# Kernel tuning notes

Hardware: AMD Instinct MI355X
Metric: run time of the kernel (lower is better)

Reference implementation:

```python
import jax, jax.numpy as jnp
import numpy as np
import math

D_MODEL = 768
N_HEAD = 12
SEQ_LEN = 2048
BATCH = 4


def setup_inputs() -> dict:
    key = jax.random.key(0)
    ks = jax.random.split(key, 5)
    x = jax.random.normal(ks[0], (BATCH, SEQ_LEN, D_MODEL), dtype=jnp.float32)
    s = 1.0 / math.sqrt(D_MODEL)
    W_attn = jax.random.uniform(ks[1], (D_MODEL, 3 * D_MODEL), minval=-s, maxval=s, dtype=jnp.float32)
    b_attn = jax.random.uniform(ks[2], (3 * D_MODEL,), minval=-s, maxval=s, dtype=jnp.float32)
    W_proj = jax.random.uniform(ks[3], (D_MODEL, D_MODEL), minval=-s, maxval=s, dtype=jnp.float32)
    b_proj = jax.random.uniform(ks[4], (D_MODEL,), minval=-s, maxval=s, dtype=jnp.float32)
    return {"x": x, "W_attn": W_attn, "b_attn": b_attn, "W_proj": W_proj, "b_proj": b_proj}


def reference(x, W_attn, b_attn, W_proj, b_proj):
    B, T, C = x.shape
    H = N_HEAD
    hd = C // H
    qkv = x @ W_attn + b_attn  # [B,T,3C]
    q, k, v = jnp.split(qkv, 3, axis=-1)
    # [B,H,T,hd]
    q = q.reshape(B, T, H, hd).transpose(0, 2, 1, 3)
    k = k.reshape(B, T, H, hd).transpose(0, 2, 1, 3)
    v = v.reshape(B, T, H, hd).transpose(0, 2, 1, 3)
    att = jnp.einsum('bhqd,bhkd->bhqk', q, k) * (1.0 / math.sqrt(hd))  # [B,H,T,T]
    causal = jnp.tril(jnp.ones((T, T), dtype=bool))
    att = jnp.where(causal[None, None, :, :], att, -jnp.inf)
    att = jax.nn.softmax(att, axis=-1)
    # attn_pdrop = resid_pdrop = 0.0 -> dropout is identity
    y = jnp.einsum('bhqk,bhkd->bhqd', att, v)  # [B,H,T,hd]
    y = y.transpose(0, 2, 1, 3).reshape(B, T, C)
    return y @ W_proj + b_proj
```

## Files before the change

kernel.cpp:

```cpp
#include <hip/hip_runtime.h>
#include <hip/hip_bf16.h>
#include <math.h>

#define D_MODEL 768
#define N_HEAD  12
#define SEQ     2048
#define BATCH   4
#define HD      64
#define BH      (BATCH*N_HEAD)

typedef __bf16 bf16;
typedef __bf16 bf16x4 __attribute__((ext_vector_type(4)));
typedef __bf16 bf16x8 __attribute__((ext_vector_type(8)));
typedef float  f32x4  __attribute__((ext_vector_type(4)));
typedef float  f32x16 __attribute__((ext_vector_type(16)));
typedef unsigned int u32;

__device__ __forceinline__ f32x4 mfma16(bf16x8 a, bf16x8 b, f32x4 c) {
    return __builtin_amdgcn_mfma_f32_16x16x32_bf16(a, b, c, 0, 0, 0);
}
__device__ __forceinline__ f32x16 mfma32(bf16x8 a, bf16x8 b, f32x16 c) {
    return __builtin_amdgcn_mfma_f32_32x32x16_bf16(a, b, c, 0, 0, 0);
}

__device__ __forceinline__ void gload16(const void* g, void* l) {
    __builtin_amdgcn_global_load_lds((const __attribute__((address_space(1))) u32*)g,
                                     (__attribute__((address_space(3))) u32*)l, 16, 0, 0);
}

__global__ void cvt_bf16(const float* __restrict__ in, bf16* __restrict__ out, int n) {
    int i = (blockIdx.x * blockDim.x + threadIdx.x) * 4;
    if (i < n) {
        float4 v = *(const float4*)(in + i);
        bf16x4 o;
        o[0] = (bf16)v.x; o[1] = (bf16)v.y; o[2] = (bf16)v.z; o[3] = (bf16)v.w;
        *(bf16x4*)(out + i) = o;
    }
}

__global__ __launch_bounds__(256)
void transpose_cvt(const float* __restrict__ in, bf16* __restrict__ out, int R, int C) {
    __shared__ float tile[64][65];
    int tid = threadIdx.x;
    int tr = blockIdx.y * 64, tc = blockIdx.x * 64;
    int r0 = tid >> 4, c0 = (tid & 15) * 4;
    #pragma unroll
    for (int i = 0; i < 4; ++i) {
        float4 v = *(const float4*)&in[(long)(tr + r0 + i * 16) * C + tc + c0];
        tile[r0 + i * 16][c0 + 0] = v.x;
        tile[r0 + i * 16][c0 + 1] = v.y;
        tile[r0 + i * 16][c0 + 2] = v.z;
        tile[r0 + i * 16][c0 + 3] = v.w;
    }
    __syncthreads();
    int orr = (tid & 15) * 4;
    #pragma unroll
    for (int i = 0; i < 4; ++i) {
        int oc = (tid >> 4) + i * 16;
        bf16x4 o;
        #pragma unroll
        for (int j = 0; j < 4; ++j) o[j] = (bf16)tile[orr + j][oc];
        *(bf16x4*)&out[(long)(tc + oc) * R + tr + orr] = o;
    }
}

template<int MODE>
__global__ __launch_bounds__(256)
void gemm_bt(const bf16* __restrict__ A, const bf16* __restrict__ Bt,
             const float* __restrict__ bias,
             bf16* __restrict__ qo, bf16* __restrict__ ko, bf16* __restrict__ vto,
             float* __restrict__ outf,
             int M, int N, int K) {
    __shared__ bf16 As[128 * 32];
    __shared__ bf16 Bs[128 * 32];
    int tid = threadIdx.x;
    int wave = tid >> 6, lane = tid & 63;
    int wr = wave >> 1, wc = wave & 1;
    int lq = lane >> 4, lc = lane & 15;
    int mbase = blockIdx.x * 128, nbase = blockIdx.y * 128;
    int srow = wave * 32 + (lane >> 2), scol = (lane & 3) * 8;
    const bf16* aS = A  + (long)(mbase + srow) * K + scol;
    const bf16* bS = Bt + (long)(nbase + srow) * K + scol;
    char* AsB = (char*)As + wave * 2048;
    char* BsB = (char*)Bs + wave * 2048;
    f32x4 acc[4][4] = {};
    for (int kt = 0; kt < K; kt += 32) {
        gload16(aS + kt,                AsB);
        gload16(aS + 16 * (long)K + kt, AsB + 1024);
        gload16(bS + kt,                BsB);
        gload16(bS + 16 * (long)K + kt, BsB + 1024);
        __syncthreads();
        bf16x8 af[4], bfr[4];
        #pragma unroll
        for (int mf = 0; mf < 4; ++mf)
            af[mf]  = *(const bf16x8*)((char*)As + (wr * 64 + mf * 16 + lc) * 64 + lq * 16);
        #pragma unroll
        for (int nf = 0; nf < 4; ++nf)
            bfr[nf] = *(const bf16x8*)((char*)Bs + (wc * 64 + nf * 16 + lc) * 64 + lq * 16);
        __builtin_amdgcn_s_setprio(1);
        #pragma unroll
        for (int mf = 0; mf < 4; ++mf)
            #pragma unroll
            for (int nf = 0; nf < 4; ++nf)
                acc[mf][nf] = mfma16(af[mf], bfr[nf], acc[mf][nf]);
        __builtin_amdgcn_s_setprio(0);
        __syncthreads();
    }
    #pragma unroll
    for (int mf = 0; mf < 4; ++mf) {
        #pragma unroll
        for (int nf = 0; nf < 4; ++nf) {
            int n = nbase + wc * 64 + nf * 16 + lc;
            float bv = bias[n];
            int m0 = mbase + wr * 64 + mf * 16 + lq * 4;
            if (MODE == 0) {
                int sect = n / 768, cc = n % 768;
                int h = cc >> 6, d = cc & 63;
                int b = m0 >> 11, t0 = m0 & 2047;
                long bh = (long)b * N_HEAD + h;
                if (sect == 0) {
                    #pragma unroll
                    for (int r = 0; r < 4; ++r)
                        qo[(bh * SEQ + t0 + r) * HD + d] = (bf16)((acc[mf][nf][r] + bv) * 0.18033688f);
                } else if (sect == 1) {
                    #pragma unroll
                    for (int r = 0; r < 4; ++r)
                        ko[(bh * SEQ + t0 + r) * HD + d] = (bf16)(acc[mf][nf][r] + bv);
                } else {
                    bf16x4 o;
                    #pragma unroll
                    for (int r = 0; r < 4; ++r) o[r] = (bf16)(acc[mf][nf][r] + bv);
                    *(bf16x4*)&vto[(bh * HD + d) * SEQ + t0] = o;
                }
            } else {
                #pragma unroll
                for (int r = 0; r < 4; ++r)
                    outf[(long)(m0 + r) * N + n] = acc[mf][nf][r] + bv;
            }
        }
    }
}

__global__ __launch_bounds__(256, 3)
void attn_kernel(const bf16* __restrict__ qg, const bf16* __restrict__ kg,
                 const bf16* __restrict__ vtg, bf16* __restrict__ yg) {
    __shared__ bf16 Ks[64 * 64];
    __shared__ bf16 Vs[64 * 64];
    int tid = threadIdx.x;
    int wave = tid >> 6, lane = tid & 63;
    int q5 = lane & 31, h = lane >> 5;
    int bh = blockIdx.x;
    int t = gridDim.y - 1 - blockIdx.y;
    int b = bh / N_HEAD, hh = bh % N_HEAD;
    int wp = wave >> 1;
    int myt     = 2 * t + wp;
    int mytiles = myt + 1;
    int nkt     = 2 * t + 2;
    long koff = (long)bh * SEQ * HD;
    long voff = (long)bh * HD * SEQ;
    int qrow = myt * 64 + (wave & 1) * 32 + q5;

    bf16x8 qf[4];
    #pragma unroll
    for (int s = 0; s < 4; ++s)
        qf[s] = *(const bf16x8*)&qg[koff + (long)qrow * HD + s * 16 + h * 8];

    f32x16 y0 = {}, y1 = {};
    float m2 = -INFINITY, lsum = 0.f;

    int srow0 = wave * 16 + (lane >> 3);
    int scolsw = ((lane & 7) ^ (lane >> 3)) << 3;
    int rsw = lane & 7;
    const char* KsC = (const char*)Ks;
    const char* VsC = (const char*)Vs;

    for (int kt = 0; kt < nkt; ++kt) {
        int k0 = kt * 64;
        {
            char* KsB = (char*)Ks + wave * 2048;
            char* VsB = (char*)Vs + wave * 2048;
            gload16(kg + koff + (long)(k0 + srow0) * HD + scolsw,       KsB);
            gload16(kg + koff + (long)(k0 + srow0 + 8) * HD + scolsw,   KsB + 1024);
            gload16(vtg + voff + (long)srow0 * SEQ + k0 + scolsw,       VsB);
            gload16(vtg + voff + (long)(srow0 + 8) * SEQ + k0 + scolsw, VsB + 1024);
        }
        __syncthreads();
        if (kt < mytiles) {
            f32x16 s0 = {}, s1 = {};
            __builtin_amdgcn_s_setprio(1);
            #pragma unroll
            for (int s = 0; s < 4; ++s) {
                bf16x8 kf0 = *(const bf16x8*)(KsC + q5 * 128        + (((s * 2 + h) ^ rsw) << 4));
                bf16x8 kf1 = *(const bf16x8*)(KsC + (32 + q5) * 128 + (((s * 2 + h) ^ rsw) << 4));
                s0 = mfma32(kf0, qf[s], s0);
                s1 = mfma32(kf1, qf[s], s1);
            }
            __builtin_amdgcn_s_setprio(0);
            if (kt == mytiles - 1) {
                #pragma unroll
                for (int r = 0; r < 16; ++r) {
                    int ka = k0 + (r & 3) + 8 * (r >> 2) + 4 * h;
                    if (ka > qrow)      s0[r] = -INFINITY;
                    if (ka + 32 > qrow) s1[r] = -INFINITY;
                }
            }
            float pmax = s0[0];
            #pragma unroll
            for (int r = 1; r < 16; ++r) pmax = fmaxf(pmax, s0[r]);
            #pragma unroll
            for (int r = 0; r < 16; ++r) pmax = fmaxf(pmax, s1[r]);
            pmax = fmaxf(pmax, __shfl_xor(pmax, 32));
            if (!__all(pmax <= m2 + 11.5f)) {
                float mnew = fmaxf(m2, pmax);
                float sc = __builtin_amdgcn_exp2f(m2 - mnew);
                #pragma unroll
                for (int r = 0; r < 16; ++r) { y0[r] *= sc; y1[r] *= sc; }
                lsum *= sc;
                m2 = mnew;
            }
            float psum = 0.f;
            u32 d0a[4], d1a[4], d0b[4], d1b[4];
            #pragma unroll
            for (int m = 0; m < 4; ++m) {
                union { bf16x4 v; u32 w[2]; } pa, pb;
                #pragma unroll
                for (int rr = 0; rr < 4; ++rr) {
                    float p0 = __builtin_amdgcn_exp2f(s0[4 * m + rr] - m2);
                    float p1 = __builtin_amdgcn_exp2f(s1[4 * m + rr] - m2);
                    psum += p0 + p1;
                    pa.v[rr] = (bf16)p0; pb.v[rr] = (bf16)p1;
                }
                d0a[m] = pa.w[0]; d1a[m] = pa.w[1];
                d0b[m] = pb.w[0]; d1b[m] = pb.w[1];
            }
            psum += __shfl_xor(psum, 32);
            lsum += psum;
            u32 e0a[4], e1a[4], e0b[4], e1b[4];
            #pragma unroll
            for (int m = 0; m < 4; ++m) {
                e0a[m] = __shfl_xor(d0a[m], 32); e1a[m] = __shfl_xor(d1a[m], 32);
                e0b[m] = __shfl_xor(d0b[m], 32); e1b[m] = __shfl_xor(d1b[m], 32);
            }
            __builtin_amdgcn_s_setprio(1);
            #pragma unroll
            for (int s = 0; s < 4; ++s) {
                int m0 = 2 * (s & 1), m1 = m0 + 1;
                union { bf16x8 v; u32 w[4]; } fr;
                if (s < 2) {
                    fr.w[0] = h ? e0a[m1] : d0a[m0];
                    fr.w[1] = h ? e1a[m1] : d1a[m0];
                    fr.w[2] = h ? d0a[m1] : e0a[m0];
                    fr.w[3] = h ? d1a[m1] : e1a[m0];
                } else {
                    fr.w[0] = h ? e0b[m1] : d0b[m0];
                    fr.w[1] = h ? e1b[m1] : d1b[m0];
                    fr.w[2] = h ? d0b[m1] : e0b[m0];
                    fr.w[3] = h ? d1b[m1] : e1b[m0];
                }
                bf16x8 v0 = *(const bf16x8*)(VsC + q5 * 128        + (((s * 2 + h) ^ rsw) << 4));
                bf16x8 v1 = *(const bf16x8*)(VsC + (32 + q5) * 128 + (((s * 2 + h) ^ rsw) << 4));
                y0 = mfma32(v0, fr.v, y0);
                y1 = mfma32(v1, fr.v, y1);
            }
            __builtin_amdgcn_s_setprio(0);
        }
        __syncthreads();
    }

    float inv = 1.f / lsum;
    long rowoff = ((long)b * SEQ + qrow) * D_MODEL + (long)hh * HD;
    #pragma unroll
    for (int m = 0; m < 4; ++m) {
        bf16x4 o0, o1;
        #pragma unroll
        for (int rr = 0; rr < 4; ++rr) {
            o0[rr] = (bf16)(y0[4 * m + rr] * inv);
            o1[rr] = (bf16)(y1[4 * m + rr] * inv);
        }
        *(bf16x4*)&yg[rowoff + 8 * m + 4 * h]      = o0;
        *(bf16x4*)&yg[rowoff + 32 + 8 * m + 4 * h] = o1;
    }
}

extern "C" void kernel_launch(void* const* d_in, const int* in_sizes, int n_in,
                              void* d_out, int out_size, void* d_ws, size_t ws_size,
                              hipStream_t stream) {
    const float* x      = (const float*)d_in[0];
    const float* W_attn = (const float*)d_in[1];
    const float* b_attn = (const float*)d_in[2];
    const float* W_proj = (const float*)d_in[3];
    const float* b_proj = (const float*)d_in[4];
    float* out = (float*)d_out;

    char* ws = (char*)d_ws;
    size_t off = 0;
    auto alloc = [&](size_t bytes) { void* p = ws + off; off += (bytes + 255) & ~255ULL; return p; };
    bf16* xb  = (bf16*)alloc(8192ULL * 768 * 2);
    bf16* Wab = (bf16*)alloc(2304ULL * 768 * 2);
    bf16* Wpb = (bf16*)alloc(768ULL * 768 * 2);
    bf16* qb_ = (bf16*)alloc((size_t)BH * SEQ * HD * 2);
    bf16* kb_ = (bf16*)alloc((size_t)BH * SEQ * HD * 2);
    bf16* vtb = (bf16*)alloc((size_t)BH * SEQ * HD * 2);
    bf16* yb  = (bf16*)alloc(8192ULL * 768 * 2);

    hipLaunchKernelGGL(cvt_bf16, dim3((8192 * 768 / 4 + 255) / 256), dim3(256), 0, stream,
                       x, xb, 8192 * 768);
    hipLaunchKernelGGL(transpose_cvt, dim3(2304 / 64, 768 / 64), dim3(256), 0, stream,
                       W_attn, Wab, 768, 2304);
    hipLaunchKernelGGL(transpose_cvt, dim3(768 / 64, 768 / 64), dim3(256), 0, stream,
                       W_proj, Wpb, 768, 768);
    hipLaunchKernelGGL((gemm_bt<0>), dim3(64, 18), dim3(256), 0, stream,
                       xb, Wab, b_attn, qb_, kb_, vtb, (float*)nullptr, 8192, 2304, 768);
    hipLaunchKernelGGL(attn_kernel, dim3(48, 16), dim3(256), 0, stream,
                       qb_, kb_, vtb, yb);
    hipLaunchKernelGGL((gemm_bt<1>), dim3(64, 6), dim3(256), 0, stream,
                       yb, Wpb, b_proj, (bf16*)nullptr, (bf16*)nullptr, (bf16*)nullptr, out, 8192, 768, 768);
}
```

Before: 212.8 us.

## Split attention KV range across wave pairs with in-block softmax merge

Each block now handles one 64-row query tile instead of two. The two wave pairs split the causal key range in half, each with its own K/V shared buffers, and their partial softmax states (max, sum, accumulator) are merged through shared memory at the end. The grid doubles and launch bounds rise to 5 blocks per SM. This balances causal work within a block and improves occupancy, at the cost of more shared memory per block, an extra merge pass, and some idle iterations when the halves are uneven.

```diff
diff --git a/kernel.cpp b/kernel.cpp
--- a/kernel.cpp
+++ b/kernel.cpp
@@ -141,24 +141,25 @@
     }
 }
 
-__global__ __launch_bounds__(256, 3)
+__global__ __launch_bounds__(256, 5)
 void attn_kernel(const bf16* __restrict__ qg, const bf16* __restrict__ kg,
                  const bf16* __restrict__ vtg, bf16* __restrict__ yg) {
-    __shared__ bf16 Ks[64 * 64];
-    __shared__ bf16 Vs[64 * 64];
+    __shared__ __align__(16) bf16 KV[4][64 * 64];
     int tid = threadIdx.x;
     int wave = tid >> 6, lane = tid & 63;
     int q5 = lane & 31, h = lane >> 5;
     int bh = blockIdx.x;
-    int t = gridDim.y - 1 - blockIdx.y;
+    int tau = gridDim.y - 1 - blockIdx.y;
     int b = bh / N_HEAD, hh = bh % N_HEAD;
-    int wp = wave >> 1;
-    int myt     = 2 * t + wp;
-    int mytiles = myt + 1;
-    int nkt     = 2 * t + 2;
+    int rh = wave & 1, wp = wave >> 1;
+    int nkt  = tau + 1;
+    int half = nkt >> 1;
+    int base = wp ? half : 0;
+    int cnt  = wp ? nkt - half : half;
+    int maxc = nkt - half;
     long koff = (long)bh * SEQ * HD;
     long voff = (long)bh * HD * SEQ;
-    int qrow = myt * 64 + (wave & 1) * 32 + q5;
+    int qrow = tau * 64 + rh * 32 + q5;
 
     bf16x8 qf[4];
     #pragma unroll
@@ -168,24 +169,28 @@
     f32x16 y0 = {}, y1 = {};
     float m2 = -INFINITY, lsum = 0.f;
 
-    int srow0 = wave * 16 + (lane >> 3);
+    int srow0 = rh * 32 + (lane >> 3);
     int scolsw = ((lane & 7) ^ (lane >> 3)) << 3;
     int rsw = lane & 7;
-    const char* KsC = (const char*)Ks;
-    const char* VsC = (const char*)Vs;
-
-    for (int kt = 0; kt < nkt; ++kt) {
-        int k0 = kt * 64;
-        {
-            char* KsB = (char*)Ks + wave * 2048;
-            char* VsB = (char*)Vs + wave * 2048;
-            gload16(kg + koff + (long)(k0 + srow0) * HD + scolsw,       KsB);
-            gload16(kg + koff + (long)(k0 + srow0 + 8) * HD + scolsw,   KsB + 1024);
-            gload16(vtg + voff + (long)srow0 * SEQ + k0 + scolsw,       VsB);
-            gload16(vtg + voff + (long)(srow0 + 8) * SEQ + k0 + scolsw, VsB + 1024);
+    const char* KsC = (const char*)KV[2 * wp];
+    const char* VsC = (const char*)KV[2 * wp + 1];
+
+    for (int i = 0; i < maxc; ++i) {
+        int tt = base + i;
+        bool active = i < cnt;
+        if (active) {
+            int k0 = tt * 64;
+            char* KsB = (char*)KV[2 * wp]     + rh * 4096;
+            char* VsB = (char*)KV[2 * wp + 1] + rh * 4096;
+            #pragma unroll
+            for (int j = 0; j < 4; ++j) {
+                gload16(kg + koff + (long)(k0 + srow0 + j * 8) * HD + scolsw,  KsB + j * 1024);
+                gload16(vtg + voff + (long)(srow0 + j * 8) * SEQ + k0 + scolsw, VsB + j * 1024);
+            }
         }
         __syncthreads();
-        if (kt < mytiles) {
+        if (active) {
+            int k0 = tt * 64;
             f32x16 s0 = {}, s1 = {};
             __builtin_amdgcn_s_setprio(1);
             #pragma unroll
@@ -196,7 +201,7 @@
                 s1 = mfma32(kf1, qf[s], s1);
             }
             __builtin_amdgcn_s_setprio(0);
-            if (kt == mytiles - 1) {
+            if (tt == nkt - 1) {
                 #pragma unroll
                 for (int r = 0; r < 16; ++r) {
                     int ka = k0 + (r & 3) + 8 * (r >> 2) + 4 * h;
@@ -267,18 +272,32 @@
         __syncthreads();
     }
 
-    float inv = 1.f / lsum;
-    long rowoff = ((long)b * SEQ + qrow) * D_MODEL + (long)hh * HD;
-    #pragma unroll
-    for (int m = 0; m < 4; ++m) {
-        bf16x4 o0, o1;
-        #pragma unroll
-        for (int rr = 0; rr < 4; ++rr) {
-            o0[rr] = (bf16)(y0[4 * m + rr] * inv);
-            o1[rr] = (bf16)(y1[4 * m + rr] * inv);
+    float* ms = (float*)&KV[0][0];
+    int slot = (rh * 64 + lane) * 36;
+    if (wp) {
+        ms[slot] = m2; ms[slot + 1] = lsum;
+        #pragma unroll
+        for (int r = 0; r < 16; ++r) { ms[slot + 4 + r] = y0[r]; ms[slot + 20 + r] = y1[r]; }
+    }
+    __syncthreads();
+    if (!wp) {
+        float mB = ms[slot], lB = ms[slot + 1];
+        float mf = fmaxf(m2, mB);
+        float a  = __builtin_amdgcn_exp2f(m2 - mf);
+        float bb = __builtin_amdgcn_exp2f(mB - mf);
+        float inv = 1.f / (lsum * a + lB * bb);
+        long rowoff = ((long)b * SEQ + qrow) * D_MODEL + (long)hh * HD;
+        #pragma unroll
+        for (int m = 0; m < 4; ++m) {
+            bf16x4 o0, o1;
+            #pragma unroll
+            for (int rr = 0; rr < 4; ++rr) {
+                o0[rr] = (bf16)((y0[4 * m + rr] * a + ms[slot + 4 + 4 * m + rr] * bb) * inv);
+                o1[rr] = (bf16)((y1[4 * m + rr] * a + ms[slot + 20 + 4 * m + rr] * bb) * inv);
+            }
+            *(bf16x4*)&yg[rowoff + 8 * m + 4 * h]      = o0;
+            *(bf16x4*)&yg[rowoff + 32 + 8 * m + 4 * h] = o1;
         }
-        *(bf16x4*)&yg[rowoff + 8 * m + 4 * h]      = o0;
-        *(bf16x4*)&yg[rowoff + 32 + 8 * m + 4 * h] = o1;
     }
 }
 
@@ -311,7 +330,7 @@
                        W_proj, Wpb, 768, 768);
     hipLaunchKernelGGL((gemm_bt<0>), dim3(64, 18), dim3(256), 0, stream,
                        xb, Wab, b_attn, qb_, kb_, vtb, (float*)nullptr, 8192, 2304, 768);
-    hipLaunchKernelGGL(attn_kernel, dim3(48, 16), dim3(256), 0, stream,
+    hipLaunchKernelGGL(attn_kernel, dim3(48, 32), dim3(256), 0, stream,
                        qb_, kb_, vtb, yb);
     hipLaunchKernelGGL((gemm_bt<1>), dim3(64, 6), dim3(256), 0, stream,
                        yb, Wpb, b_proj, (bf16*)nullptr, (bf16*)nullptr, (bf16*)nullptr, out, 8192, 768, 768);
```

Result: slower. 224.5 us (+5.5%).
